# Kernel optimization log

Hardware: AMD Instinct MI355X
Metric: run time of the kernel (lower is better)

## Reference

```python
import jax, jax.numpy as jnp
import numpy as np


def setup_inputs() -> dict:
    key = jax.random.key(0)
    ks = jax.random.split(key, 5)
    T, B, C, H, K = 2048, 8, 1024, 16, 7
    s = 1.0 / np.sqrt(C)
    return {
        "x": jax.random.normal(ks[0], (T, B, C), dtype=jnp.float32),
        "w_weight": jax.random.normal(ks[1], (H * K, C), dtype=jnp.float32) * s,
        "glu_w": jax.random.normal(ks[2], (2 * H, C), dtype=jnp.float32) * s,
        "glu_b": jnp.zeros((2 * H,), dtype=jnp.float32),
        "out_w": jax.random.normal(ks[3], (C, C), dtype=jnp.float32) * s,
        "out_b": jnp.zeros((C,), dtype=jnp.float32),
        "padding_l": 6,
    }


def reference(x, w_weight, glu_w, glu_b, out_w, out_b, padding_l):
    # x: (T, B, C) in TBC format
    T, B, C = x.shape
    H = glu_w.shape[0] // 2
    K = w_weight.shape[0] // H
    R = C // H  # channels per head

    # GLU gate: C -> 2H, split last dim, a * sigmoid(b)  -> (T, B, H)
    g = (x @ glu_w.T + glu_b).reshape(T, B, H, 2)
    gate = g[..., 0] * jax.nn.sigmoid(g[..., 1])

    # per-position per-head kernel weights, softmax over K -> (T, B, H, K)
    w = jax.nn.softmax((x @ w_weight.T).reshape(T, B, H, K), axis=-1)

    # depthwise dynamic conv: out[t] = sum_k w[t,k] * x_pad[t + k]
    xh = x.reshape(T, B, H, R)
    xp = jnp.pad(xh, ((padding_l, K - 1 - padding_l), (0, 0), (0, 0), (0, 0)))
    conv = jnp.zeros_like(xh)
    for k in range(K):  # K is small & static; avoids (B,H,T,K,R) unfold blowup
        conv = conv + w[..., k:k + 1] * jax.lax.dynamic_slice_in_dim(xp, k, T, axis=0)

    # gate per head, merge heads, output projection
    out = (conv * gate[..., None]).reshape(T, B, C)
    return out @ out_w.T + out_b
```

## Files before the change

kernel.cpp:

```cpp
#include <hip/hip_runtime.h>
#include <hip/hip_bf16.h>
#include <stdint.h>

#define T_DIM 2048
#define B_DIM 8
#define C_DIM 1024
#define H_DIM 16
#define K_DIM 7
#define M_DIM (T_DIM * B_DIM)
#define NLOG 144
#define CW_STRIDE 128

typedef __attribute__((ext_vector_type(8))) short short8;
typedef __attribute__((ext_vector_type(4))) float floatx4;

__device__ __forceinline__ ushort f2bf(float f) {
    __hip_bfloat16 h = __float2bfloat16(f);
    return *(ushort*)&h;
}

#define S_W  ((size_t)112 * C_DIM)
#define S_G  ((size_t)32 * C_DIM)
#define S_O  ((size_t)C_DIM * C_DIM)
#define S_WG (S_W + S_G)
#define S_CVT (S_WG + S_O)

__global__ __launch_bounds__(256) void cvt_w_kernel(
    const float* __restrict__ w_weight, const float* __restrict__ glu_w,
    const float* __restrict__ out_w,
    ushort* __restrict__ wb, ushort* __restrict__ Wb)
{
    size_t gid = ((size_t)blockIdx.x * 256 + threadIdx.x) * 4;
    const float* src; ushort* dst; size_t off;
    if (gid < S_W)            { src = w_weight; dst = wb;       off = gid; }
    else if (gid < S_WG)      { src = glu_w;    dst = wb + S_W; off = gid - S_W; }
    else                      { src = out_w;    dst = Wb;       off = gid - S_WG; }
    float4 v = *(const float4*)(src + off);
    ushort4 o; o.x = f2bf(v.x); o.y = f2bf(v.y); o.z = f2bf(v.z); o.w = f2bf(v.w);
    *(ushort4*)(dst + off) = o;
}

__global__ __launch_bounds__(256) void logits_kernel(
    const float* __restrict__ x,
    const ushort* __restrict__ wb,
    const float* __restrict__ glu_b,
    float* __restrict__ cw)
{
    __shared__ __align__(16) ushort Bs[2][144 * 32];
    __shared__ float lsm[64][NLOG];

    const int tid = threadIdx.x;
    const int wave = tid >> 6, lane = tid & 63;
    const int fr = lane & 15, q = lane >> 4;
    const int m0 = blockIdx.x * 64;
    const int mrow = m0 + wave * 16 + fr;

    floatx4 acc[9];
#pragma unroll
    for (int j = 0; j < 9; ++j) acc[j] = (floatx4){0.f, 0.f, 0.f, 0.f};

    const float* arow = x + (size_t)mrow * C_DIM + q * 8;

    for (int i = tid; i < 576; i += 256) {
        int r = i >> 2, ch = i & 3;
        __builtin_amdgcn_global_load_lds(
            (const __attribute__((address_space(1))) void*)(wb + (size_t)r * C_DIM + ch * 8),
            (__attribute__((address_space(3))) void*)(&Bs[0][0] + i * 8), 16, 0, 0);
    }
    float4 a0 = *(const float4*)(arow);
    float4 a1 = *(const float4*)(arow + 4);
    __syncthreads();

    for (int kc = 0; kc < 32; ++kc) {
        const int buf = kc & 1;
        if (kc < 31) {
            const ushort* wsrc = wb + (kc + 1) * 32;
            for (int i = tid; i < 576; i += 256) {
                int r = i >> 2, ch = i & 3;
                __builtin_amdgcn_global_load_lds(
                    (const __attribute__((address_space(1))) void*)(wsrc + (size_t)r * C_DIM + ch * 8),
                    (__attribute__((address_space(3))) void*)(&Bs[buf ^ 1][0] + i * 8), 16, 0, 0);
            }
        }
        short8 a;
        a[0] = (short)f2bf(a0.x); a[1] = (short)f2bf(a0.y);
        a[2] = (short)f2bf(a0.z); a[3] = (short)f2bf(a0.w);
        a[4] = (short)f2bf(a1.x); a[5] = (short)f2bf(a1.y);
        a[6] = (short)f2bf(a1.z); a[7] = (short)f2bf(a1.w);
        if (kc < 31) {
            a0 = *(const float4*)(arow + (kc + 1) * 32);
            a1 = *(const float4*)(arow + (kc + 1) * 32 + 4);
        }
#pragma unroll
        for (int j = 0; j < 9; ++j) {
            short8 b = *(const short8*)(&Bs[buf][0] + ((j * 16 + fr) * 4 + q) * 8);
            acc[j] = __builtin_amdgcn_mfma_f32_16x16x32_bf16(a, b, acc[j], 0, 0, 0);
        }
        __syncthreads();
    }

#pragma unroll
    for (int j = 0; j < 9; ++j)
#pragma unroll
        for (int r = 0; r < 4; ++r)
            lsm[wave * 16 + q * 4 + r][j * 16 + fr] = acc[j][r];
    __syncthreads();

    {
        const int row = tid >> 2;
        const int hbase = (tid & 3) * 4;
        float* crow = cw + (size_t)(m0 + row) * CW_STRIDE;
#pragma unroll
        for (int hh = 0; hh < 4; ++hh) {
            const int h = hbase + hh;
            float l[K_DIM];
            float mx = -1e30f;
#pragma unroll
            for (int k = 0; k < K_DIM; ++k) { l[k] = lsm[row][h * K_DIM + k]; mx = fmaxf(mx, l[k]); }
            float s = 0.f;
#pragma unroll
            for (int k = 0; k < K_DIM; ++k) { l[k] = __expf(l[k] - mx); s += l[k]; }
            float inv = 1.f / s;
#pragma unroll
            for (int k = 0; k < K_DIM; ++k) crow[h * K_DIM + k] = l[k] * inv;
            float ga = lsm[row][112 + 2 * h] + glu_b[2 * h];
            float gb = lsm[row][113 + 2 * h] + glu_b[2 * h + 1];
            crow[112 + h] = ga * (1.f / (1.f + __expf(-gb)));
        }
    }
}

__global__ __launch_bounds__(256) void conv_kernel(
    const float* __restrict__ x,
    const float* __restrict__ cw,
    const int* __restrict__ padding_l_,
    ushort* __restrict__ y)
{
    const int lb = (blockIdx.x & 7) * 512 + (blockIdx.x >> 3);
    const int wave = threadIdx.x >> 6, lane = threadIdx.x & 63;
    const int m = lb * 4 + wave;
    const int t = m >> 3;
    const int pad = *padding_l_;
    const int h = lane >> 2;

    const float* crow = cw + (size_t)m * CW_STRIDE;
    float wt[K_DIM];
#pragma unroll
    for (int k = 0; k < K_DIM; ++k) wt[k] = crow[h * K_DIM + k];
    const float g = crow[112 + h];

    const int c0 = lane * 16;
    float av[16];
#pragma unroll
    for (int i = 0; i < 16; ++i) av[i] = 0.f;

#pragma unroll
    for (int k = 0; k < K_DIM; ++k) {
        int ts = t + k - pad;
        if (ts < 0 || ts >= T_DIM) continue;
        float wv = wt[k];
        const float4* xp = (const float4*)(x + ((size_t)m + 8 * (k - pad)) * C_DIM + c0);
        float4 u0 = xp[0], u1 = xp[1], u2 = xp[2], u3 = xp[3];
        av[0]  += wv * u0.x; av[1]  += wv * u0.y; av[2]  += wv * u0.z; av[3]  += wv * u0.w;
        av[4]  += wv * u1.x; av[5]  += wv * u1.y; av[6]  += wv * u1.z; av[7]  += wv * u1.w;
        av[8]  += wv * u2.x; av[9]  += wv * u2.y; av[10] += wv * u2.z; av[11] += wv * u2.w;
        av[12] += wv * u3.x; av[13] += wv * u3.y; av[14] += wv * u3.z; av[15] += wv * u3.w;
    }

    uint32_t o[8];
#pragma unroll
    for (int i = 0; i < 8; ++i)
        o[i] = (uint32_t)f2bf(av[2 * i] * g) | ((uint32_t)f2bf(av[2 * i + 1] * g) << 16);
    uint4* yr = (uint4*)(y + (size_t)m * C_DIM + c0);
    yr[0] = (uint4){o[0], o[1], o[2], o[3]};
    yr[1] = (uint4){o[4], o[5], o[6], o[7]};
}

__global__ __launch_bounds__(256) void out_gemm(
    const ushort* __restrict__ y,
    const ushort* __restrict__ Wb,
    const float* __restrict__ bias,
    float* __restrict__ out)
{
    __shared__ __align__(16) ushort SM[2][2][128 * 64];

    const int bn = blockIdx.x & 7;
    const int bm = blockIdx.x >> 3;
    const int m0 = bm * 128, n0 = bn * 128;
    const int tid = threadIdx.x;
    const int lane = tid & 63, wave = tid >> 6;
    const int wm = (wave >> 1) * 64, wn = (wave & 1) * 64;
    const int fr = lane & 15, q = lane >> 4;

    floatx4 acc[4][4];
#pragma unroll
    for (int i = 0; i < 4; ++i)
#pragma unroll
        for (int j = 0; j < 4; ++j) acc[i][j] = (floatx4){0.f, 0.f, 0.f, 0.f};

    auto stage = [&](int buf, int k0) {
#pragma unroll
        for (int j = 0; j < 4; ++j) {
            int idx = j * 256 + tid;
            int r = idx >> 3, cl = idx & 7;
            int ch = cl ^ (r & 7);
            __builtin_amdgcn_global_load_lds(
                (const __attribute__((address_space(1))) void*)(y + (size_t)(m0 + r) * C_DIM + k0 + ch * 8),
                (__attribute__((address_space(3))) void*)(&SM[buf][0][0] + idx * 8), 16, 0, 0);
            __builtin_amdgcn_global_load_lds(
                (const __attribute__((address_space(1))) void*)(Wb + (size_t)(n0 + r) * C_DIM + k0 + ch * 8),
                (__attribute__((address_space(3))) void*)(&SM[buf][1][0] + idx * 8), 16, 0, 0);
        }
    };

    stage(0, 0);

#pragma unroll 2
    for (int kt = 0; kt < 16; ++kt) {
        const int buf = kt & 1;
        if (kt < 15) {
            stage(buf ^ 1, (kt + 1) * 64);
            asm volatile("s_waitcnt vmcnt(8)" ::: "memory");
        } else {
            asm volatile("s_waitcnt vmcnt(0)" ::: "memory");
        }
        __builtin_amdgcn_s_barrier();
        asm volatile("" ::: "memory");

        const ushort* Ab = &SM[buf][0][0];
        const ushort* Bb = &SM[buf][1][0];
#pragma unroll
        for (int s = 0; s < 64; s += 32) {
            const int cbase = (s >> 3) + q;
            short8 a[4], b[4];
#pragma unroll
            for (int i = 0; i < 4; ++i) {
                int r = wm + i * 16 + fr;
                a[i] = *(const short8*)(Ab + r * 64 + ((cbase ^ (r & 7)) * 8));
            }
#pragma unroll
            for (int j = 0; j < 4; ++j) {
                int r = wn + j * 16 + fr;
                b[j] = *(const short8*)(Bb + r * 64 + ((cbase ^ (r & 7)) * 8));
            }
#pragma unroll
            for (int i = 0; i < 4; ++i)
#pragma unroll
                for (int j = 0; j < 4; ++j)
                    acc[i][j] = __builtin_amdgcn_mfma_f32_16x16x32_bf16(a[i], b[j], acc[i][j], 0, 0, 0);
        }

        asm volatile("" ::: "memory");
        __builtin_amdgcn_s_barrier();
        asm volatile("" ::: "memory");
    }

    float* Cs = (float*)&SM[0][0][0];
#pragma unroll
    for (int i = 0; i < 4; ++i)
#pragma unroll
        for (int j = 0; j < 4; ++j)
#pragma unroll
            for (int r = 0; r < 4; ++r)
                Cs[(wm + i * 16 + q * 4 + r) * 128 + (wn + j * 16 + fr)] = acc[i][j][r];
    __syncthreads();

    {
        const int c4 = (tid & 31) * 4;
        floatx4 bv = *(const floatx4*)(bias + n0 + c4);
#pragma unroll
        for (int rep = 0; rep < 16; ++rep) {
            int row = rep * 8 + (tid >> 5);
            floatx4 v = *(const floatx4*)(Cs + row * 128 + c4);
            v = v + bv;
            __builtin_nontemporal_store(v, (floatx4*)(out + (size_t)(m0 + row) * C_DIM + n0 + c4));
        }
    }
}

extern "C" void kernel_launch(void* const* d_in, const int* in_sizes, int n_in,
                              void* d_out, int out_size, void* d_ws, size_t ws_size,
                              hipStream_t stream) {
    const float* x        = (const float*)d_in[0];
    const float* w_weight = (const float*)d_in[1];
    const float* glu_w    = (const float*)d_in[2];
    const float* glu_b    = (const float*)d_in[3];
    const float* out_w    = (const float*)d_in[4];
    const float* out_b    = (const float*)d_in[5];
    const int* padding_l  = (const int*)d_in[6];
    float* out = (float*)d_out;

    char* ws = (char*)d_ws;
    ushort* y  = (ushort*)ws;
    ushort* wb = y + (size_t)M_DIM * C_DIM;
    ushort* Wb = wb + S_WG;
    float* cwp = (float*)(Wb + S_O);

    cvt_w_kernel<<<S_CVT / 4 / 256, 256, 0, stream>>>(w_weight, glu_w, out_w, wb, Wb);
    logits_kernel<<<M_DIM / 64, 256, 0, stream>>>(x, wb, glu_b, cwp);
    conv_kernel<<<M_DIM / 4, 256, 0, stream>>>(x, cwp, padding_l, y);
    out_gemm<<<(M_DIM / 128) * (C_DIM / 128), 256, 0, stream>>>(y, Wb, out_b, out);
}
```

Measured before the change: 234.1 us.

## Enlarge out_gemm tiles to 256x256 with triple-buffered K=32 pipeline

After: 221.5 us. 1.06x faster.

```diff
diff --git a/kernel.cpp b/kernel.cpp
--- a/kernel.cpp
+++ b/kernel.cpp
@@ -176,34 +176,36 @@
     yr[1] = (uint4){o[4], o[5], o[6], o[7]};
 }
 
-__global__ __launch_bounds__(256) void out_gemm(
+__global__ __launch_bounds__(512, 2) void out_gemm(
     const ushort* __restrict__ y,
     const ushort* __restrict__ Wb,
     const float* __restrict__ bias,
     float* __restrict__ out)
 {
-    __shared__ __align__(16) ushort SM[2][2][128 * 64];
-
-    const int bn = blockIdx.x & 7;
-    const int bm = blockIdx.x >> 3;
-    const int m0 = bm * 128, n0 = bn * 128;
+    __shared__ __align__(16) ushort SM[3][2][256 * 32];
+
+    const int orig = (blockIdx.x & 7) * 32 + (blockIdx.x >> 3);
+    const int bm = orig >> 2;
+    const int bn = orig & 3;
+    const int m0 = bm * 256, n0 = bn * 256;
     const int tid = threadIdx.x;
     const int lane = tid & 63, wave = tid >> 6;
-    const int wm = (wave >> 1) * 64, wn = (wave & 1) * 64;
+    const int wr = wave >> 2;
+    const int wc = wave & 3;
     const int fr = lane & 15, q = lane >> 4;
 
-    floatx4 acc[4][4];
-#pragma unroll
-    for (int i = 0; i < 4; ++i)
+    floatx4 acc[8][4];
+#pragma unroll
+    for (int i = 0; i < 8; ++i)
 #pragma unroll
         for (int j = 0; j < 4; ++j) acc[i][j] = (floatx4){0.f, 0.f, 0.f, 0.f};
 
     auto stage = [&](int buf, int k0) {
 #pragma unroll
-        for (int j = 0; j < 4; ++j) {
-            int idx = j * 256 + tid;
-            int r = idx >> 3, cl = idx & 7;
-            int ch = cl ^ (r & 7);
+        for (int j = 0; j < 2; ++j) {
+            int idx = j * 512 + tid;
+            int r = idx >> 2, cl = idx & 3;
+            int ch = cl ^ ((r >> 1) & 3);
             __builtin_amdgcn_global_load_lds(
                 (const __attribute__((address_space(1))) void*)(y + (size_t)(m0 + r) * C_DIM + k0 + ch * 8),
                 (__attribute__((address_space(3))) void*)(&SM[buf][0][0] + idx * 8), 16, 0, 0);
@@ -214,66 +216,58 @@
     };
 
     stage(0, 0);
-
-#pragma unroll 2
-    for (int kt = 0; kt < 16; ++kt) {
-        const int buf = kt & 1;
-        if (kt < 15) {
-            stage(buf ^ 1, (kt + 1) * 64);
-            asm volatile("s_waitcnt vmcnt(8)" ::: "memory");
-        } else {
-            asm volatile("s_waitcnt vmcnt(0)" ::: "memory");
-        }
+    stage(1, 32);
+
+    int cur = 0;
+    for (int kt = 0; kt < 32; ++kt) {
+        if (kt + 2 < 32) {
+            int stg = cur + 2; if (stg >= 3) stg -= 3;
+            stage(stg, (kt + 2) * 32);
+        }
+        if (kt < 30)       asm volatile("s_waitcnt vmcnt(8)" ::: "memory");
+        else if (kt == 30) asm volatile("s_waitcnt vmcnt(4)" ::: "memory");
+        else               asm volatile("s_waitcnt vmcnt(0)" ::: "memory");
         __builtin_amdgcn_s_barrier();
         asm volatile("" ::: "memory");
 
-        const ushort* Ab = &SM[buf][0][0];
-        const ushort* Bb = &SM[buf][1][0];
-#pragma unroll
-        for (int s = 0; s < 64; s += 32) {
-            const int cbase = (s >> 3) + q;
-            short8 a[4], b[4];
-#pragma unroll
-            for (int i = 0; i < 4; ++i) {
-                int r = wm + i * 16 + fr;
-                a[i] = *(const short8*)(Ab + r * 64 + ((cbase ^ (r & 7)) * 8));
-            }
-#pragma unroll
-            for (int j = 0; j < 4; ++j) {
-                int r = wn + j * 16 + fr;
-                b[j] = *(const short8*)(Bb + r * 64 + ((cbase ^ (r & 7)) * 8));
-            }
-#pragma unroll
-            for (int i = 0; i < 4; ++i)
-#pragma unroll
-                for (int j = 0; j < 4; ++j)
-                    acc[i][j] = __builtin_amdgcn_mfma_f32_16x16x32_bf16(a[i], b[j], acc[i][j], 0, 0, 0);
-        }
+        const ushort* Ab = &SM[cur][0][0];
+        const ushort* Bb = &SM[cur][1][0];
+        short8 a[8], b[4];
+#pragma unroll
+        for (int mf = 0; mf < 8; ++mf) {
+            int r = wr * 128 + mf * 16 + fr;
+            a[mf] = *(const short8*)(Ab + r * 32 + ((q ^ ((r >> 1) & 3)) * 8));
+        }
+#pragma unroll
+        for (int nf = 0; nf < 4; ++nf) {
+            int r = wc * 64 + nf * 16 + fr;
+            b[nf] = *(const short8*)(Bb + r * 32 + ((q ^ ((r >> 1) & 3)) * 8));
+        }
+        __builtin_amdgcn_s_setprio(1);
+#pragma unroll
+        for (int mf = 0; mf < 8; ++mf)
+#pragma unroll
+            for (int nf = 0; nf < 4; ++nf)
+                acc[mf][nf] = __builtin_amdgcn_mfma_f32_16x16x32_bf16(a[mf], b[nf], acc[mf][nf], 0, 0, 0);
+        __builtin_amdgcn_s_setprio(0);
 
         asm volatile("" ::: "memory");
         __builtin_amdgcn_s_barrier();
         asm volatile("" ::: "memory");
-    }
-
-    float* Cs = (float*)&SM[0][0][0];
-#pragma unroll
-    for (int i = 0; i < 4; ++i)
-#pragma unroll
-        for (int j = 0; j < 4; ++j)
-#pragma unroll
-            for (int r = 0; r < 4; ++r)
-                Cs[(wm + i * 16 + q * 4 + r) * 128 + (wn + j * 16 + fr)] = acc[i][j][r];
-    __syncthreads();
-
-    {
-        const int c4 = (tid & 31) * 4;
-        floatx4 bv = *(const floatx4*)(bias + n0 + c4);
-#pragma unroll
-        for (int rep = 0; rep < 16; ++rep) {
-            int row = rep * 8 + (tid >> 5);
-            floatx4 v = *(const floatx4*)(Cs + row * 128 + c4);
-            v = v + bv;
-            __builtin_nontemporal_store(v, (floatx4*)(out + (size_t)(m0 + row) * C_DIM + n0 + c4));
+        cur = (cur == 2) ? 0 : cur + 1;
+    }
+
+#pragma unroll
+    for (int nf = 0; nf < 4; ++nf) {
+        int n = n0 + wc * 64 + nf * 16 + fr;
+        float bv = bias[n];
+#pragma unroll
+        for (int mf = 0; mf < 8; ++mf) {
+#pragma unroll
+            for (int r = 0; r < 4; ++r) {
+                int m = m0 + wr * 128 + mf * 16 + q * 4 + r;
+                out[(size_t)m * C_DIM + n] = acc[mf][nf][r] + bv;
+            }
         }
     }
 }
@@ -299,5 +293,5 @@
     cvt_w_kernel<<<S_CVT / 4 / 256, 256, 0, stream>>>(w_weight, glu_w, out_w, wb, Wb);
     logits_kernel<<<M_DIM / 64, 256, 0, stream>>>(x, wb, glu_b, cwp);
     conv_kernel<<<M_DIM / 4, 256, 0, stream>>>(x, cwp, padding_l, y);
-    out_gemm<<<(M_DIM / 128) * (C_DIM / 128), 256, 0, stream>>>(y, Wb, out_b, out);
-}
+    out_gemm<<<(M_DIM / 256) * (C_DIM / 256), 512, 0, stream>>>(y, Wb, out_b, out);
+}
```
